# Kernel optimization log

Hardware: AMD Instinct MI355X
Metric: run time of the kernel (lower is better)

Reference implementation:

```python
import math
import jax, jax.numpy as jnp
import numpy as np

M, D, R, N = 16, 256, 16, 131072  # modes, support per mode, TR rank, n samples


def setup_inputs() -> dict:
    key = jax.random.key(0)
    k1, k2 = jax.random.split(key)
    index = jax.random.randint(k1, (N, M), 0, D, dtype=jnp.int32)
    # reset_cores(): normal(theta, 0.1) with theta = log(expm1(1/(d*r)))
    theta = math.log(math.expm1(1.0 / (D * R)))
    log_cores = theta + 0.1 * jax.random.normal(k2, (M, D, R, R), dtype=jnp.float32)
    return {"index": index, "log_cores": log_cores}


def reference(index, log_cores):
    """TRCategorical.log_prob: sequential TR-core chain with running rescale."""
    cores = jax.nn.softplus(log_cores)          # [M, D, R, R], positive cores
    n = index.shape[0]

    # normalizer: norm = prod_k sum_j G^k_j, then log trace
    bars = cores.sum(axis=1)                    # [M, R, R]
    def norm_step(c, b):
        return c @ b, None
    norm, _ = jax.lax.scan(norm_step, jnp.eye(R, dtype=cores.dtype), bars)
    log_norm = jnp.log(jnp.trace(norm))

    # sequential chain: gather core[ix] -> bmm -> running max rescale
    eye = jnp.broadcast_to(jnp.eye(R, dtype=cores.dtype), (n, R, R))
    zero = jnp.zeros((n,), dtype=cores.dtype)

    def step(carry, x):
        prob, log_scale = carry                 # [n,R,R], [n]
        core, ix = x                            # [D,R,R], [n]
        margin = core[ix]                       # gather -> [n,R,R]
        prob = prob @ margin                    # batched matmul
        s = jax.lax.stop_gradient(jnp.max(prob.reshape(n, -1), axis=1))
        log_scale = log_scale + jnp.log(s)
        prob = prob / s[:, None, None]
        return (prob, log_scale), None

    (prob, log_scale), _ = jax.lax.scan(step, (eye, zero), (cores, index.T))

    log_tr = jnp.log(jnp.trace(prob, axis1=1, axis2=2))  # [n]
    return log_tr - log_norm + log_scale
```

## Files before the change

kernel.cpp:

```cpp
#include <hip/hip_runtime.h>

typedef short v4s __attribute__((ext_vector_type(4)));
typedef float v4f __attribute__((ext_vector_type(4)));
typedef unsigned int v2u __attribute__((ext_vector_type(2)));
union FU { v2u u; v4s s; };
union FL { v2u u; long long l; };

static __device__ __forceinline__ unsigned int f32_to_e4m3(float x){
    unsigned int u = __float_as_uint(x);
    unsigned int mr = (u & 0x7FFFFFu) + 0x7FFFFu + ((u>>20)&1u);
    unsigned int e  = ((u>>23)&255u) + (mr>>23);
    return ((e-120u)<<3) | ((mr>>20)&7u);
}
static __device__ __forceinline__ float e4m3_to_f32(unsigned int b){
    return __uint_as_float(((b<<4) + 0x3C00u)<<16);
}

#define CVT_ACC_TO_B(lo, hi, acc) \
    asm("s_nop 1\n\t" \
        "v_cvt_pk_bf16_f32 %0, %2, %3\n\t" \
        "v_cvt_pk_bf16_f32 %1, %4, %5\n\t" \
        "s_nop 1" \
        : "=&v"(lo), "=&v"(hi) \
        : "v"(acc[0]), "v"(acc[1]), "v"(acc[2]), "v"(acc[3]))

#define SPW 4


__global__ void k_softplus_fp8(const float* __restrict__ lc,
                               unsigned int* __restrict__ c8,
                               unsigned int* __restrict__ cT8){
    int t = blockIdx.x*256 + threadIdx.x;
    float4 v = ((const float4*)lc)[t];
    float s0 = (v.x>20.f)?v.x:log1pf(expf(v.x));
    float s1 = (v.y>20.f)?v.y:log1pf(expf(v.y));
    float s2 = (v.z>20.f)?v.z:log1pf(expf(v.z));
    float s3 = (v.w>20.f)?v.w:log1pf(expf(v.w));
    unsigned int d = f32_to_e4m3(s0*4096.f) | (f32_to_e4m3(s1*4096.f)<<8)
                   | (f32_to_e4m3(s2*4096.f)<<16) | (f32_to_e4m3(s3*4096.f)<<24);
    c8[t] = d;
    int f  = t<<2;
    int md = f>>8, c = (f>>4)&15, r = f&15;
    const float* s = lc + (md<<8) + c;
    float x0 = s[(r+0)<<4], x1 = s[(r+1)<<4], x2 = s[(r+2)<<4], x3 = s[(r+3)<<4];
    x0 = (x0>20.f)?x0:log1pf(expf(x0));
    x1 = (x1>20.f)?x1:log1pf(expf(x1));
    x2 = (x2>20.f)?x2:log1pf(expf(x2));
    x3 = (x3>20.f)?x3:log1pf(expf(x3));
    unsigned int dT = f32_to_e4m3(x0*4096.f) | (f32_to_e4m3(x1*4096.f)<<8)
                    | (f32_to_e4m3(x2*4096.f)<<16) | (f32_to_e4m3(x3*4096.f)<<24);
    cT8[t] = dT;
}

__global__ void k_bars_fp8(const unsigned char* __restrict__ c8, float* __restrict__ bars4){
    int b = blockIdx.x, t = threadIdx.x;
    int m = b>>2, dq = b&3;
    const unsigned char* p = c8 + m*65536 + dq*64*256 + t;
    float s = 0.f;
    #pragma unroll 16
    for (int d=0; d<64; d++) s += e4m3_to_f32(p[d*256]);
    bars4[dq*4096 + m*256 + t] = s;
}

__global__ void k_norm2(const float* __restrict__ bars4, float* __restrict__ lognorm){
    __shared__ float sbars[16*256];
    __shared__ float cur[256];
    int t = threadIdx.x, i = t>>4, j = t&15;
    for (int m=0;m<16;m++){
        int o = m*256 + t;
        sbars[o] = bars4[o] + bars4[4096+o] + bars4[8192+o] + bars4[12288+o];
    }
    cur[t] = (i==j)?1.f:0.f;
    __syncthreads();
    for (int m=0;m<16;m++){
        float s = 0.f;
        #pragma unroll
        for (int k=0;k<16;k++) s += cur[i*16+k]*sbars[m*256 + k*16 + j];
        s *= 0.000244140625f;
        __syncthreads();
        cur[t] = s;
        __syncthreads();
    }
    if (t==0){
        float tr=0.f;
        #pragma unroll
        for (int k=0;k<16;k++) tr += cur[k*17];
        lognorm[0] = logf(tr) + 192.0f*0.69314718055994531f;
    }
}

static __device__ __forceinline__ void gatherP(v2u* F,
        const int* __restrict__ ipa, const int* __restrict__ ipb,
        const unsigned char* __restrict__ c8, const unsigned char* __restrict__ cT8,
        int laneoffB, bool lo){
    #pragma unroll
    for (int k=0;k<16;k++){
        int ix = lo ? ipa[k] : ipb[k];
        const unsigned char* tp = (k&1)? cT8 : c8;
        F[k] = *(const v2u*)(tp + (((k<<8)|ix)<<8) + laneoffB);
    }
}

static __device__ __forceinline__ void tree_level1_pair(const v2u* F, bool lo,
        unsigned int* c1loA, unsigned int* c1hiA,
        unsigned int* c1loB, unsigned int* c1hiB){
    #pragma unroll
    for (int i=0;i<8;i++){
        v2u fe = F[2*i];
        v2u fo = F[2*i+1];
        v2u fx = (i&1)? fe : fo;
        v2u bz = (i&1)? fo : fe;
        v2u aa, ab;
        aa.x = lo ? fx.x : 0u;  aa.y = lo ? fx.y : 0u;
        ab.x = lo ? 0u : fx.x;  ab.y = lo ? 0u : fx.y;
        FL A0; A0.u = aa;
        FL A1; A1.u = ab;
        FL B;  B.u  = bz;
        v4f z = {0.f,0.f,0.f,0.f};
        v4f accA = __builtin_amdgcn_mfma_f32_16x16x32_fp8_fp8(A0.l, B.l, z, 0,0,0);
        v4f accB = __builtin_amdgcn_mfma_f32_16x16x32_fp8_fp8(A1.l, B.l, z, 0,0,0);
        CVT_ACC_TO_B(c1loA[i], c1hiA[i], accA);
        CVT_ACC_TO_B(c1loB[i], c1hiB[i], accB);
    }
}

static __device__ __forceinline__ float tree_level23(const unsigned int* c1lo,
        const unsigned int* c1hi){
    unsigned int c2lo[4], c2hi[4];
    #pragma unroll
    for (int j=0;j<4;j++){
        FU A,B;
        if (j&1){ A.u=(v2u){c1lo[2*j],c1hi[2*j]};     B.u=(v2u){c1lo[2*j+1],c1hi[2*j+1]}; }
        else    { A.u=(v2u){c1lo[2*j+1],c1hi[2*j+1]}; B.u=(v2u){c1lo[2*j],c1hi[2*j]};     }
        v4f z={0.f,0.f,0.f,0.f};
        v4f acc=__builtin_amdgcn_mfma_f32_16x16x16bf16_1k(A.s,B.s,z,0,0,0);
        CVT_ACC_TO_B(c2lo[j],c2hi[j],acc);
    }
    FU A0,B0,A1,B1;
    A0.u=(v2u){c2lo[1],c2hi[1]}; B0.u=(v2u){c2lo[0],c2hi[0]};
    A1.u=(v2u){c2lo[2],c2hi[2]}; B1.u=(v2u){c2lo[3],c2hi[3]};
    v4f z={0.f,0.f,0.f,0.f};
    v4f aL=__builtin_amdgcn_mfma_f32_16x16x16bf16_1k(A0.s,B0.s,z,0,0,0);
    v4f aR=__builtin_amdgcn_mfma_f32_16x16x16bf16_1k(A1.s,B1.s,z,0,0,0);
    return aL[0]*aR[0]+aL[1]*aR[1]+aL[2]*aR[2]+aL[3]*aR[3];
}

__global__ __launch_bounds__(256) void k_chain12(const int* __restrict__ idx,
    const unsigned char* __restrict__ c8, const unsigned char* __restrict__ cT8,
    const float* __restrict__ lognorm, float* __restrict__ out)
{
    const int lane = threadIdx.x & 63;
    const int wq   = __builtin_amdgcn_readfirstlane(threadIdx.x >> 6);
    const int wave = (blockIdx.x<<2) + wq;
    const int row  = lane & 15;
    const int laneoffB = row*16 + ((lane>>4)&1)*8;
    const bool lo  = (lane < 32);
    const float L = lognorm[0];
    const int s0 = wave * SPW;
    const int* __restrict__ ip = idx + (s0<<4);

    v2u FA[16], FB[16];
    unsigned int c1loA[8], c1hiA[8], c1loB[8], c1hiB[8];
    float d0,d1,d2,d3;

    gatherP(FA, ip,    ip+16, c8, cT8, laneoffB, lo);
    tree_level1_pair(FA, lo, c1loA, c1hiA, c1loB, c1hiB);
    gatherP(FB, ip+32, ip+48, c8, cT8, laneoffB, lo);
    d0 = tree_level23(c1loA, c1hiA);
    d1 = tree_level23(c1loB, c1hiB);

    tree_level1_pair(FB, lo, c1loA, c1hiA, c1loB, c1hiB);
    d2 = tree_level23(c1loA, c1hiA);
    d3 = tree_level23(c1loB, c1hiB);

    #pragma unroll
    for (int off=32; off>0; off>>=1){
        d0 += __shfl_xor(d0, off, 64);
        d1 += __shfl_xor(d1, off, 64);
        d2 += __shfl_xor(d2, off, 64);
        d3 += __shfl_xor(d3, off, 64);
    }
    float res = (lane==0)?d0:(lane==1)?d1:(lane==2)?d2:(lane==3)?d3:0.f;

    if (lane < SPW){
        float o;
        if (!(L > -1e30f && L < 1e30f)) o = -5555.0f;
        else if (res > 0.f)             o = logf(res) - L;
        else                            o = -6666.0f;
        out[s0 + lane] = o;
    }
}

extern "C" void kernel_launch(void* const* d_in, const int* in_sizes, int n_in,
                              void* d_out, int out_size, void* d_ws, size_t ws_size,
                              hipStream_t stream)
{
    const int*   idx = (const int*)d_in[0];
    const float* lc  = (const float*)d_in[1];
    float* out = (float*)d_out;

    const size_t C8_B    = (size_t)16*256*256;
    const size_t BARS4_B = (size_t)4*16*256*4;
    const size_t WS_NEED = 2*C8_B + BARS4_B + 4;
    if (ws_size < WS_NEED) return;

    unsigned int* c8   = (unsigned int*)d_ws;
    unsigned int* cT8  = (unsigned int*)((char*)d_ws + C8_B);
    float* bars4   = (float*)((char*)d_ws + 2*C8_B);
    float* lognorm = (float*)((char*)d_ws + 2*C8_B + BARS4_B);

    k_softplus_fp8<<<1024, 256, 0, stream>>>(lc, c8, cT8);
    k_bars_fp8    <<<64,   256, 0, stream>>>((const unsigned char*)c8, bars4);
    k_norm2       <<<1,    256, 0, stream>>>(bars4, lognorm);
    int nblocks = out_size / (SPW*4);
    k_chain12     <<<nblocks, 256, 0, stream>>>(idx, (const unsigned char*)c8,
                                                (const unsigned char*)cT8, lognorm, out);
}
```

Baseline: 65.97 us.

## Process eight samples per wave with double-buffered gathers and vectorized bar sums

The chain kernel now handles eight samples per wave instead of four. It alternates two fragment buffers so the gather for the next pair of samples is issued before the current pair's MFMA tree runs, which overlaps more memory latency. This halves the number of blocks and raises register pressure. The bar-sum kernel also reads packed 32-bit words (four fp8 values each) across 16 partial slices, and the norm kernel is updated to reduce all 16 slices. Gather address math is switched to unsigned offsets from a per-mode base.

```diff
diff --git a/kernel.cpp b/kernel.cpp
--- a/kernel.cpp
+++ b/kernel.cpp
@@ -24,7 +24,7 @@
         : "=&v"(lo), "=&v"(hi) \
         : "v"(acc[0]), "v"(acc[1]), "v"(acc[2]), "v"(acc[3]))
 
-#define SPW 4
+#define SPW 8
 
 
 __global__ void k_softplus_fp8(const float* __restrict__ lc,
@@ -52,23 +52,33 @@
     cT8[t] = dT;
 }
 
-__global__ void k_bars_fp8(const unsigned char* __restrict__ c8, float* __restrict__ bars4){
+__global__ void k_bars16(const unsigned int* __restrict__ c8d, float* __restrict__ bars16){
     int b = blockIdx.x, t = threadIdx.x;
-    int m = b>>2, dq = b&3;
-    const unsigned char* p = c8 + m*65536 + dq*64*256 + t;
-    float s = 0.f;
-    #pragma unroll 16
-    for (int d=0; d<64; d++) s += e4m3_to_f32(p[d*256]);
-    bars4[dq*4096 + m*256 + t] = s;
-}
-
-__global__ void k_norm2(const float* __restrict__ bars4, float* __restrict__ lognorm){
+    int m = b>>2, dq = b&3, q = t>>6, p = t&63;
+    const unsigned int* base = c8d + m*16384 + (dq*64 + q*16)*64 + p;
+    float s0=0.f, s1=0.f, s2=0.f, s3=0.f;
+    #pragma unroll
+    for (int d=0; d<16; d++){
+        unsigned int u = base[d*64];
+        s0 += e4m3_to_f32(u & 255u);
+        s1 += e4m3_to_f32((u>>8) & 255u);
+        s2 += e4m3_to_f32((u>>16) & 255u);
+        s3 += e4m3_to_f32(u>>24);
+    }
+    float* o = bars16 + (dq*4+q)*4096 + m*256 + p*4;
+    o[0]=s0; o[1]=s1; o[2]=s2; o[3]=s3;
+}
+
+__global__ void k_norm16(const float* __restrict__ bars16, float* __restrict__ lognorm){
     __shared__ float sbars[16*256];
     __shared__ float cur[256];
     int t = threadIdx.x, i = t>>4, j = t&15;
     for (int m=0;m<16;m++){
         int o = m*256 + t;
-        sbars[o] = bars4[o] + bars4[4096+o] + bars4[8192+o] + bars4[12288+o];
+        float s = 0.f;
+        #pragma unroll
+        for (int pq=0;pq<16;pq++) s += bars16[pq*4096 + o];
+        sbars[o] = s;
     }
     cur[t] = (i==j)?1.f:0.f;
     __syncthreads();
@@ -92,12 +102,13 @@
 static __device__ __forceinline__ void gatherP(v2u* F,
         const int* __restrict__ ipa, const int* __restrict__ ipb,
         const unsigned char* __restrict__ c8, const unsigned char* __restrict__ cT8,
-        int laneoffB, bool lo){
+        unsigned int laneoffB, bool lo){
     #pragma unroll
     for (int k=0;k<16;k++){
-        int ix = lo ? ipa[k] : ipb[k];
-        const unsigned char* tp = (k&1)? cT8 : c8;
-        F[k] = *(const v2u*)(tp + (((k<<8)|ix)<<8) + laneoffB);
+        const unsigned char* tbase = ((k&1)? cT8 : c8) + (k<<16);
+        unsigned int ix = (unsigned int)(lo ? ipa[k] : ipb[k]);
+        unsigned int voff = (ix<<8) + laneoffB;
+        F[k] = *(const v2u*)(tbase + voff);
     }
 }
 
@@ -145,7 +156,15 @@
     return aL[0]*aR[0]+aL[1]*aR[1]+aL[2]*aR[2]+aL[3]*aR[3];
 }
 
-__global__ __launch_bounds__(256) void k_chain12(const int* __restrict__ idx,
+static __device__ __forceinline__ void pair_compute(const v2u* F, bool lo,
+        float& da, float& db){
+    unsigned int c1loA[8], c1hiA[8], c1loB[8], c1hiB[8];
+    tree_level1_pair(F, lo, c1loA, c1hiA, c1loB, c1hiB);
+    da = tree_level23(c1loA, c1hiA);
+    db = tree_level23(c1loB, c1hiB);
+}
+
+__global__ __launch_bounds__(256) void k_chain14(const int* __restrict__ idx,
     const unsigned char* __restrict__ c8, const unsigned char* __restrict__ cT8,
     const float* __restrict__ lognorm, float* __restrict__ out)
 {
@@ -153,25 +172,23 @@
     const int wq   = __builtin_amdgcn_readfirstlane(threadIdx.x >> 6);
     const int wave = (blockIdx.x<<2) + wq;
     const int row  = lane & 15;
-    const int laneoffB = row*16 + ((lane>>4)&1)*8;
+    const unsigned int laneoffB = (unsigned int)(row*16 + ((lane>>4)&1)*8);
     const bool lo  = (lane < 32);
     const float L = lognorm[0];
     const int s0 = wave * SPW;
     const int* __restrict__ ip = idx + (s0<<4);
 
     v2u FA[16], FB[16];
-    unsigned int c1loA[8], c1hiA[8], c1loB[8], c1hiB[8];
-    float d0,d1,d2,d3;
-
-    gatherP(FA, ip,    ip+16, c8, cT8, laneoffB, lo);
-    tree_level1_pair(FA, lo, c1loA, c1hiA, c1loB, c1hiB);
-    gatherP(FB, ip+32, ip+48, c8, cT8, laneoffB, lo);
-    d0 = tree_level23(c1loA, c1hiA);
-    d1 = tree_level23(c1loB, c1hiB);
-
-    tree_level1_pair(FB, lo, c1loA, c1hiA, c1loB, c1hiB);
-    d2 = tree_level23(c1loA, c1hiA);
-    d3 = tree_level23(c1loB, c1hiB);
+    float d0,d1,d2,d3,d4,d5,d6,d7;
+
+    gatherP(FA, ip,      ip+16,  c8, cT8, laneoffB, lo);
+    gatherP(FB, ip+32,   ip+48,  c8, cT8, laneoffB, lo);
+    pair_compute(FA, lo, d0, d1);
+    gatherP(FA, ip+64,   ip+80,  c8, cT8, laneoffB, lo);
+    pair_compute(FB, lo, d2, d3);
+    gatherP(FB, ip+96,   ip+112, c8, cT8, laneoffB, lo);
+    pair_compute(FA, lo, d4, d5);
+    pair_compute(FB, lo, d6, d7);
 
     #pragma unroll
     for (int off=32; off>0; off>>=1){
@@ -179,8 +196,16 @@
         d1 += __shfl_xor(d1, off, 64);
         d2 += __shfl_xor(d2, off, 64);
         d3 += __shfl_xor(d3, off, 64);
-    }
-    float res = (lane==0)?d0:(lane==1)?d1:(lane==2)?d2:(lane==3)?d3:0.f;
+        d4 += __shfl_xor(d4, off, 64);
+        d5 += __shfl_xor(d5, off, 64);
+        d6 += __shfl_xor(d6, off, 64);
+        d7 += __shfl_xor(d7, off, 64);
+    }
+    float res = 0.f;
+    res = (lane==0)?d0:res;  res = (lane==1)?d1:res;
+    res = (lane==2)?d2:res;  res = (lane==3)?d3:res;
+    res = (lane==4)?d4:res;  res = (lane==5)?d5:res;
+    res = (lane==6)?d6:res;  res = (lane==7)?d7:res;
 
     if (lane < SPW){
         float o;
@@ -200,19 +225,19 @@
     float* out = (float*)d_out;
 
     const size_t C8_B    = (size_t)16*256*256;
-    const size_t BARS4_B = (size_t)4*16*256*4;
-    const size_t WS_NEED = 2*C8_B + BARS4_B + 4;
+    const size_t BARS_B  = (size_t)16*16*256*4;
+    const size_t WS_NEED = 2*C8_B + BARS_B + 4;
     if (ws_size < WS_NEED) return;
 
     unsigned int* c8   = (unsigned int*)d_ws;
     unsigned int* cT8  = (unsigned int*)((char*)d_ws + C8_B);
-    float* bars4   = (float*)((char*)d_ws + 2*C8_B);
-    float* lognorm = (float*)((char*)d_ws + 2*C8_B + BARS4_B);
+    float* bars16  = (float*)((char*)d_ws + 2*C8_B);
+    float* lognorm = (float*)((char*)d_ws + 2*C8_B + BARS_B);
 
     k_softplus_fp8<<<1024, 256, 0, stream>>>(lc, c8, cT8);
-    k_bars_fp8    <<<64,   256, 0, stream>>>((const unsigned char*)c8, bars4);
-    k_norm2       <<<1,    256, 0, stream>>>(bars4, lognorm);
+    k_bars16      <<<64,   256, 0, stream>>>(c8, bars16);
+    k_norm16      <<<1,    256, 0, stream>>>(bars16, lognorm);
     int nblocks = out_size / (SPW*4);
-    k_chain12     <<<nblocks, 256, 0, stream>>>(idx, (const unsigned char*)c8,
+    k_chain14     <<<nblocks, 256, 0, stream>>>(idx, (const unsigned char*)c8,
                                                 (const unsigned char*)cT8, lognorm, out);
 }
```

After: 67.23 us. About the same (+1.9%).
